# Kernel tuning notes

Hardware: AMD Instinct MI355X
Metric: run time of the kernel (lower is better)

## Reference

```python
import jax, jax.numpy as jnp
import numpy as np

PAD = 0
V, D = 50000, 300
MUS = np.array([-0.9, -0.7, -0.5, -0.3, -0.1, 0.1, 0.3, 0.5, 0.7, 0.9, 1.0], dtype=np.float32)
SIGMAS = np.array([0.1] * 10 + [0.001], dtype=np.float32)


def setup_inputs() -> dict:
    key = jax.random.key(0)
    k1, k2, k3, k4, k5, k6, k7 = jax.random.split(key, 7)
    B, Q, T = 256, 16, 1024
    return {
        "posdoc": jax.random.randint(k1, (B, T), 0, V),
        "negdoc": jax.random.randint(k2, (B, T), 0, V),
        "query": jax.random.randint(k3, (B, Q), 0, V),
        "query_idf": jax.random.normal(k4, (B, Q), dtype=jnp.float32),
        "emb": jax.random.normal(k5, (V, D), dtype=jnp.float32) * 0.1,
        "mus": jnp.asarray(MUS),
        "sigmas": jnp.asarray(SIGMAS),
        "W": jax.random.normal(k6, (11, 1), dtype=jnp.float32) * 0.3,
        "b": jax.random.normal(k7, (1,), dtype=jnp.float32) * 0.01,
    }


def _get_score(doc_tok, query_tok, emb, mus, sigmas, W, b):
    q = emb[query_tok]                                    # [B,Q,D]
    d = emb[doc_tok]                                      # [B,T,D]
    qn = q / (jnp.linalg.norm(q, axis=-1, keepdims=True) + 1e-9)
    dn = d / (jnp.linalg.norm(d, axis=-1, keepdims=True) + 1e-9)
    sim = jnp.einsum('bqd,btd->bqt', qn, dn)              # cosine simmat [B,Q,T]
    pair_mask = (query_tok != PAD)[:, :, None] & (doc_tok != PAD)[:, None, :]
    sim = sim * pair_mask                                 # zero out pad pairs
    # RBF kernel bank: [B,K,Q,T]
    diff = sim[:, None, :, :] - mus[None, :, None, None]
    k = jnp.exp(-0.5 * diff * diff / (sigmas[None, :, None, None] ** 2))
    doc_k = jnp.sum(k, axis=3)                            # [B,K,Q]
    qmask = jnp.sum(sim, axis=2) != 0.0                   # [B,Q]
    log_k = jnp.where(qmask[:, None, :], jnp.log(doc_k + 1e-6), 0.0)
    query_k = jnp.sum(log_k, axis=2)                      # [B,K]
    return (query_k @ W + b)[:, 0]                        # [B]


def reference(posdoc, negdoc, query, query_idf, emb, mus, sigmas, W, b):
    pos = _get_score(posdoc, query, emb, mus, sigmas, W, b)
    neg = _get_score(negdoc, query, emb, mus, sigmas, W, b)
    return jnp.stack([pos, neg], axis=1)                  # [B,2]
```

## Files before the change

### kernel.cpp

```cpp
#include <hip/hip_runtime.h>
#include <math.h>

#define BQ 16
#define TT 1024
#define DD 300
#define KK 11
#define ND4 75
#define KPAD 320
#define QSTR 328

typedef unsigned short u16;
typedef __bf16 bf16x8 __attribute__((ext_vector_type(8)));
typedef float f32x4 __attribute__((ext_vector_type(4)));

__device__ __forceinline__ u16 f2bf(float f) {
    unsigned u = __float_as_uint(f);
    u = (u + 0x7fffu + ((u >> 16) & 1u)) >> 16;
    return (u16)u;
}

__global__ __launch_bounds__(256) void knrm_norm_table(
    const float* __restrict__ emb, u16* __restrict__ table, int V)
{
    const int tid = threadIdx.x;
    const int sub = tid & 15;
    const int row = blockIdx.x * 16 + (tid >> 4);
    if (row >= V) return;

    const float4* __restrict__ src = (const float4*)(emb + (size_t)row * DD);
    float4 v[5];
    float ssq = 0.f;
    #pragma unroll
    for (int it = 0; it < 5; ++it) {
        int j = sub + 16 * it;
        if (j < ND4) {
            v[it] = src[j];
            ssq += v[it].x * v[it].x + v[it].y * v[it].y
                 + v[it].z * v[it].z + v[it].w * v[it].w;
        } else {
            v[it] = make_float4(0.f, 0.f, 0.f, 0.f);
        }
    }
    #pragma unroll
    for (int off = 8; off; off >>= 1) ssq += __shfl_xor(ssq, off, 16);
    const float inv = (row == 0) ? 0.f : 1.f / (sqrtf(ssq) + 1e-9f);

    ushort4* __restrict__ dst = (ushort4*)(table + (size_t)row * KPAD);
    #pragma unroll
    for (int it = 0; it < 5; ++it) {
        int j = sub + 16 * it;
        ushort4 o;
        o.x = f2bf(v[it].x * inv);
        o.y = f2bf(v[it].y * inv);
        o.z = f2bf(v[it].z * inv);
        o.w = f2bf(v[it].w * inv);
        dst[j] = o;
    }
}

__global__ __launch_bounds__(256, 6) void knrm_mfma(
    const int* __restrict__ posdoc, const int* __restrict__ negdoc,
    const int* __restrict__ query,
    const u16* __restrict__ table,
    const float* __restrict__ mus, const float* __restrict__ sigmas,
    float* __restrict__ part)
{
    __shared__ __align__(16) u16 qsm[BQ * QSTR];
    __shared__ float red[4][BQ][12];

    const int bid   = blockIdx.x;
    const int pair  = bid >> 3;
    const int chunk = bid & 7;
    const int bb    = pair >> 1;
    const int* __restrict__ doc = (pair & 1) ? negdoc : posdoc;
    const int tid  = threadIdx.x;
    const int lane = tid & 63;
    const int wave = tid >> 6;
    const int quad = lane >> 4;
    const int m    = lane & 15;

    {
        int row = tid >> 4;
        int qt  = query[bb * BQ + row];
        const ushort4* src = (const ushort4*)(table + (size_t)qt * KPAD);
        ushort4* dstrow = (ushort4*)(qsm + row * QSTR);
        #pragma unroll
        for (int c = tid & 15; c < KPAD / 4; c += 16) dstrow[c] = src[c];
    }
    __syncthreads();

    const int tbase = bb * TT + chunk * 128 + wave * 32 + m;
    const int dtok0 = doc[tbase];
    const int dtok1 = doc[tbase + 16];
    const u16* brow0 = table + (size_t)dtok0 * KPAD + quad * 8;
    const u16* brow1 = table + (size_t)dtok1 * KPAD + quad * 8;
    const u16* arow  = qsm + m * QSTR + quad * 8;

    f32x4 acc0 = {0.f, 0.f, 0.f, 0.f};
    f32x4 acc1 = {0.f, 0.f, 0.f, 0.f};
    #pragma unroll 2
    for (int ks = 0; ks < KPAD / 32; ++ks) {
        bf16x8 a  = *(const bf16x8*)(arow  + ks * 32);
        bf16x8 b0 = *(const bf16x8*)(brow0 + ks * 32);
        bf16x8 b1 = *(const bf16x8*)(brow1 + ks * 32);
        acc0 = __builtin_amdgcn_mfma_f32_16x16x32_bf16(a, b0, acc0, 0, 0, 0);
        acc1 = __builtin_amdgcn_mfma_f32_16x16x32_bf16(a, b1, acc1, 0, 0, 0);
    }

    float muk[KK], ck[KK];
    #pragma unroll
    for (int k = 0; k < KK; ++k) {
        muk[k] = mus[k];
        float sg = sigmas[k];
        ck[k] = -0.5f * 1.44269504088896f / (sg * sg);
    }

    #pragma unroll
    for (int r = 0; r < 4; ++r) {
        float s0 = acc0[r], s1 = acc1[r];
        float vals[12];
        vals[11] = s0 + s1;
        #pragma unroll
        for (int k = 0; k < KK; ++k) {
            float d0 = s0 - muk[k], d1 = s1 - muk[k];
            vals[k] = __builtin_amdgcn_exp2f(ck[k] * d0 * d0)
                    + __builtin_amdgcn_exp2f(ck[k] * d1 * d1);
        }
        #pragma unroll
        for (int off = 8; off; off >>= 1)
            #pragma unroll
            for (int v = 0; v < 12; ++v)
                vals[v] += __shfl_down(vals[v], off, 16);
        if (m == 0) {
            int q = quad * 4 + r;
            #pragma unroll
            for (int v = 0; v < 12; ++v) red[wave][q][v] = vals[v];
        }
    }
    __syncthreads();

    if (tid < 192) {
        int v = tid >> 4, q = tid & 15;
        float sum = red[0][q][v] + red[1][q][v] + red[2][q][v] + red[3][q][v];
        part[((size_t)bid * 12 + v) * BQ + q] = sum;
    }
}

__global__ __launch_bounds__(256) void knrm_partial(
    const int* __restrict__ posdoc, const int* __restrict__ negdoc,
    const int* __restrict__ query,
    const float* __restrict__ emb,
    const float* __restrict__ mus, const float* __restrict__ sigmas,
    float* __restrict__ ws)
{
    __shared__ __align__(16) float qs[BQ * DD];
    __shared__ float qscale[BQ];

    const int bid   = blockIdx.x;
    const int pair  = bid >> 2;
    const int chunk = bid & 3;
    const int bb    = pair >> 1;
    const int sel   = pair & 1;
    const int* __restrict__ doc = sel ? negdoc : posdoc;
    const int tid  = threadIdx.x;
    const int lane = tid & 63;
    const int wave = tid >> 6;

    float4* qs4 = (float4*)qs;
    for (int idx = tid; idx < BQ * ND4; idx += 256) {
        int q   = idx / ND4;
        int c   = idx - q * ND4;
        int tok = query[bb * BQ + q];
        qs4[idx] = ((const float4*)(emb + (size_t)tok * DD))[c];
    }
    __syncthreads();
    {
        int q = tid >> 4, sub = tid & 15;
        float ssq = 0.f;
        for (int i = sub; i < DD; i += 16) { float v = qs[q * DD + i]; ssq += v * v; }
        #pragma unroll
        for (int off = 8; off; off >>= 1) ssq += __shfl_down(ssq, off, 16);
        if (sub == 0) {
            int tok = query[bb * BQ + q];
            qscale[q] = (tok == 0) ? 0.f : 1.f / (sqrtf(ssq) + 1e-9f);
        }
    }
    __syncthreads();
    for (int idx = tid; idx < BQ * ND4; idx += 256) {
        int q = idx / ND4;
        float sc = qscale[q];
        float4 v = qs4[idx];
        v.x *= sc; v.y *= sc; v.z *= sc; v.w *= sc;
        qs4[idx] = v;
    }
    __syncthreads();

    const int tok = doc[bb * TT + chunk * 256 + tid];
    const float4* __restrict__ rowp = (const float4*)(emb + (size_t)tok * DD);
    float acc[BQ];
    #pragma unroll
    for (int q = 0; q < BQ; ++q) acc[q] = 0.f;
    float dss = 0.f;
    #pragma unroll 5
    for (int d4 = 0; d4 < ND4; ++d4) {
        float4 dv = rowp[d4];
        dss += dv.x * dv.x + dv.y * dv.y + dv.z * dv.z + dv.w * dv.w;
        #pragma unroll
        for (int q = 0; q < BQ; ++q) {
            float4 qv = qs4[q * ND4 + d4];
            acc[q] += dv.x * qv.x + dv.y * qv.y + dv.z * qv.z + dv.w * qv.w;
        }
    }
    const float invd = (tok == 0) ? 0.f : 1.f / (sqrtf(dss) + 1e-9f);

    float muk[KK], ck[KK];
    #pragma unroll
    for (int k = 0; k < KK; ++k) {
        muk[k] = mus[k];
        float sg = sigmas[k];
        ck[k] = -0.5f * 1.44269504088896f / (sg * sg);
    }
    __syncthreads();
    float* red = qs;
    const int grp = wave * 4 + (lane >> 4);
    const bool wr = (lane & 15) == 0;
    for (int q = 0; q < BQ; ++q) {
        float s = acc[q] * invd;
        float vals[12];
        vals[11] = s;
        #pragma unroll
        for (int k = 0; k < KK; ++k) {
            float d = s - muk[k];
            vals[k] = __builtin_amdgcn_exp2f(ck[k] * d * d);
        }
        #pragma unroll
        for (int off = 8; off; off >>= 1)
            #pragma unroll
            for (int v = 0; v < 12; ++v)
                vals[v] += __shfl_down(vals[v], off, 16);
        if (wr) {
            #pragma unroll
            for (int v = 0; v < 12; ++v) red[(grp * BQ + q) * 12 + v] = vals[v];
        }
    }
    __syncthreads();
    if (tid < 192) {
        int v = tid >> 4, q = tid & 15;
        float sum = 0.f;
        #pragma unroll
        for (int g = 0; g < 16; ++g) sum += red[(g * BQ + q) * 12 + v];
        ws[((size_t)(pair * 4 + chunk) * 12 + v) * BQ + q] = sum;
    }
}

__global__ __launch_bounds__(192) void knrm_final(
    const float* __restrict__ part,
    const float* __restrict__ Wv, const float* __restrict__ bv,
    float* __restrict__ out, int nchunk)
{
    __shared__ float dock[12 * BQ];
    __shared__ float lsum[KK];
    const int pair = blockIdx.x;
    const int tid  = threadIdx.x;
    {
        int v = tid >> 4, q = tid & 15;
        float sum = 0.f;
        for (int c = 0; c < nchunk; ++c)
            sum += part[((size_t)(pair * nchunk + c) * 12 + v) * BQ + q];
        dock[v * BQ + q] = sum;
    }
    __syncthreads();
    if (tid < 176) {
        int k = tid >> 4, q = tid & 15;
        float qm = dock[11 * BQ + q];
        float lv = (qm != 0.0f) ? logf(dock[k * BQ + q] + 1e-6f) : 0.f;
        #pragma unroll
        for (int off = 8; off; off >>= 1) lv += __shfl_down(lv, off, 16);
        if (q == 0) lsum[k] = lv;
    }
    __syncthreads();
    if (tid == 0) {
        float sc = bv[0];
        #pragma unroll
        for (int k = 0; k < KK; ++k) sc += lsum[k] * Wv[k];
        out[pair] = sc;
    }
}

extern "C" void kernel_launch(void* const* d_in, const int* in_sizes, int n_in,
                              void* d_out, int out_size, void* d_ws, size_t ws_size,
                              hipStream_t stream) {
    const int*   posdoc = (const int*)  d_in[0];
    const int*   negdoc = (const int*)  d_in[1];
    const int*   query  = (const int*)  d_in[2];
    const float* emb    = (const float*)d_in[4];
    const float* mus    = (const float*)d_in[5];
    const float* sigmas = (const float*)d_in[6];
    const float* Wv     = (const float*)d_in[7];
    const float* bv     = (const float*)d_in[8];
    float* out = (float*)d_out;

    const int V = in_sizes[4] / DD;
    const size_t table_bytes = (size_t)V * KPAD * sizeof(u16);
    const size_t part_bytes  = (size_t)512 * 8 * 12 * BQ * sizeof(float);

    if (ws_size >= table_bytes + part_bytes) {
        u16*   table = (u16*)d_ws;
        float* part  = (float*)((char*)d_ws + table_bytes);
        knrm_norm_table<<<dim3((V + 15) / 16), dim3(256), 0, stream>>>(emb, table, V);
        knrm_mfma<<<dim3(512 * 8), dim3(256), 0, stream>>>(
            posdoc, negdoc, query, table, mus, sigmas, part);
        knrm_final<<<dim3(512), dim3(192), 0, stream>>>(part, Wv, bv, out, 8);
    } else {
        float* part = (float*)d_ws;
        knrm_partial<<<dim3(512 * 4), dim3(256), 0, stream>>>(
            posdoc, negdoc, query, emb, mus, sigmas, part);
        knrm_final<<<dim3(512), dim3(192), 0, stream>>>(part, Wv, bv, out, 4);
    }
}
```

Before: 168.7 us.

## Process more tokens per block and accumulate kernel sums in registers

Each block now covers 512 document tokens instead of 128. Every wave loops over four token-pair tiles, reuses the query tile held in LDS, and accumulates the RBF kernel sums in registers before a single shuffle reduction. This cuts the grid from 4096 to 1024 blocks, which reduces repeated query-row loads into LDS, the shuffle/LDS reductions, and the partial-sum traffic to the final kernel. In exchange, register pressure rises (launch bounds lowered to 4 waves per SIMD), and there are fewer blocks for 256 CUs to hide gather latency with.

```diff
diff --git a/kernel.cpp b/kernel.cpp
--- a/kernel.cpp
+++ b/kernel.cpp
@@ -8,6 +8,7 @@
 #define ND4 75
 #define KPAD 320
 #define QSTR 328
+#define NCH 2
 
 typedef unsigned short u16;
 typedef __bf16 bf16x8 __attribute__((ext_vector_type(8)));
@@ -58,7 +59,7 @@
     }
 }
 
-__global__ __launch_bounds__(256, 6) void knrm_mfma(
+__global__ __launch_bounds__(256, 4) void knrm_mfma(
     const int* __restrict__ posdoc, const int* __restrict__ negdoc,
     const int* __restrict__ query,
     const u16* __restrict__ table,
@@ -69,8 +70,8 @@
     __shared__ float red[4][BQ][12];
 
     const int bid   = blockIdx.x;
-    const int pair  = bid >> 3;
-    const int chunk = bid & 7;
+    const int pair  = bid >> 1;
+    const int chunk = bid & 1;
     const int bb    = pair >> 1;
     const int* __restrict__ doc = (pair & 1) ? negdoc : posdoc;
     const int tid  = threadIdx.x;
@@ -87,25 +88,11 @@
         #pragma unroll
         for (int c = tid & 15; c < KPAD / 4; c += 16) dstrow[c] = src[c];
     }
-    __syncthreads();
-
-    const int tbase = bb * TT + chunk * 128 + wave * 32 + m;
-    const int dtok0 = doc[tbase];
-    const int dtok1 = doc[tbase + 16];
-    const u16* brow0 = table + (size_t)dtok0 * KPAD + quad * 8;
-    const u16* brow1 = table + (size_t)dtok1 * KPAD + quad * 8;
-    const u16* arow  = qsm + m * QSTR + quad * 8;
-
-    f32x4 acc0 = {0.f, 0.f, 0.f, 0.f};
-    f32x4 acc1 = {0.f, 0.f, 0.f, 0.f};
-    #pragma unroll 2
-    for (int ks = 0; ks < KPAD / 32; ++ks) {
-        bf16x8 a  = *(const bf16x8*)(arow  + ks * 32);
-        bf16x8 b0 = *(const bf16x8*)(brow0 + ks * 32);
-        bf16x8 b1 = *(const bf16x8*)(brow1 + ks * 32);
-        acc0 = __builtin_amdgcn_mfma_f32_16x16x32_bf16(a, b0, acc0, 0, 0, 0);
-        acc1 = __builtin_amdgcn_mfma_f32_16x16x32_bf16(a, b1, acc1, 0, 0, 0);
-    }
+
+    const int tbase = bb * TT + chunk * 512 + wave * 128 + m;
+    int toks[8];
+    #pragma unroll
+    for (int t = 0; t < 8; ++t) toks[t] = doc[tbase + t * 16];
 
     float muk[KK], ck[KK];
     #pragma unroll
@@ -115,26 +102,54 @@
         ck[k] = -0.5f * 1.44269504088896f / (sg * sg);
     }
 
+    __syncthreads();
+
+    const u16* arow = qsm + m * QSTR + quad * 8;
+
+    float vacc[12][4];
+    #pragma unroll
+    for (int v = 0; v < 12; ++v)
+        #pragma unroll
+        for (int r = 0; r < 4; ++r) vacc[v][r] = 0.f;
+
+    #pragma unroll
+    for (int tp = 0; tp < 4; ++tp) {
+        const u16* brow0 = table + (size_t)toks[2 * tp]     * KPAD + quad * 8;
+        const u16* brow1 = table + (size_t)toks[2 * tp + 1] * KPAD + quad * 8;
+        f32x4 acc0 = {0.f, 0.f, 0.f, 0.f};
+        f32x4 acc1 = {0.f, 0.f, 0.f, 0.f};
+        #pragma unroll
+        for (int ks = 0; ks < KPAD / 32; ++ks) {
+            bf16x8 a  = *(const bf16x8*)(arow  + ks * 32);
+            bf16x8 b0 = *(const bf16x8*)(brow0 + ks * 32);
+            bf16x8 b1 = *(const bf16x8*)(brow1 + ks * 32);
+            acc0 = __builtin_amdgcn_mfma_f32_16x16x32_bf16(a, b0, acc0, 0, 0, 0);
+            acc1 = __builtin_amdgcn_mfma_f32_16x16x32_bf16(a, b1, acc1, 0, 0, 0);
+        }
+        #pragma unroll
+        for (int r = 0; r < 4; ++r) {
+            float s0 = acc0[r], s1 = acc1[r];
+            vacc[11][r] += s0 + s1;
+            #pragma unroll
+            for (int k = 0; k < KK; ++k) {
+                float d0 = s0 - muk[k], d1 = s1 - muk[k];
+                vacc[k][r] += __builtin_amdgcn_exp2f(ck[k] * d0 * d0)
+                            + __builtin_amdgcn_exp2f(ck[k] * d1 * d1);
+            }
+        }
+    }
+
     #pragma unroll
     for (int r = 0; r < 4; ++r) {
-        float s0 = acc0[r], s1 = acc1[r];
-        float vals[12];
-        vals[11] = s0 + s1;
-        #pragma unroll
-        for (int k = 0; k < KK; ++k) {
-            float d0 = s0 - muk[k], d1 = s1 - muk[k];
-            vals[k] = __builtin_amdgcn_exp2f(ck[k] * d0 * d0)
-                    + __builtin_amdgcn_exp2f(ck[k] * d1 * d1);
-        }
         #pragma unroll
         for (int off = 8; off; off >>= 1)
             #pragma unroll
             for (int v = 0; v < 12; ++v)
-                vals[v] += __shfl_down(vals[v], off, 16);
+                vacc[v][r] += __shfl_down(vacc[v][r], off, 16);
         if (m == 0) {
             int q = quad * 4 + r;
             #pragma unroll
-            for (int v = 0; v < 12; ++v) red[wave][q][v] = vals[v];
+            for (int v = 0; v < 12; ++v) red[wave][q][v] = vacc[v][r];
         }
     }
     __syncthreads();
@@ -302,15 +317,15 @@
 
     const int V = in_sizes[4] / DD;
     const size_t table_bytes = (size_t)V * KPAD * sizeof(u16);
-    const size_t part_bytes  = (size_t)512 * 8 * 12 * BQ * sizeof(float);
+    const size_t part_bytes  = (size_t)512 * NCH * 12 * BQ * sizeof(float);
 
     if (ws_size >= table_bytes + part_bytes) {
         u16*   table = (u16*)d_ws;
         float* part  = (float*)((char*)d_ws + table_bytes);
         knrm_norm_table<<<dim3((V + 15) / 16), dim3(256), 0, stream>>>(emb, table, V);
-        knrm_mfma<<<dim3(512 * 8), dim3(256), 0, stream>>>(
+        knrm_mfma<<<dim3(512 * NCH), dim3(256), 0, stream>>>(
             posdoc, negdoc, query, table, mus, sigmas, part);
-        knrm_final<<<dim3(512), dim3(192), 0, stream>>>(part, Wv, bv, out, 8);
+        knrm_final<<<dim3(512), dim3(192), 0, stream>>>(part, Wv, bv, out, NCH);
     } else {
         float* part = (float*)d_ws;
         knrm_partial<<<dim3(512 * 4), dim3(256), 0, stream>>>(
```

After: 162.2 us. -3.9%, faster.
